# Kernel tuning notes

Measured on AMD Instinct MI355X. Metric: run time of the kernel, lower is better.

The kernel has to match this reference:

```python
import jax, jax.numpy as jnp
import numpy as np

N_NODES = 50000
N_EDGES = 800000
D = 128
BN_EPS = 1e-5

def setup_inputs() -> dict:
    key = jax.random.key(0)
    k1, k2, k3, k4, k5 = jax.random.split(key, 5)
    features = jax.random.normal(k1, (N_NODES, D), dtype=jnp.float32)
    W = jax.random.normal(k2, (D, D), dtype=jnp.float32) * (1.0 / np.sqrt(D))
    b = jax.random.normal(k3, (D,), dtype=jnp.float32) * 0.01
    gamma = jnp.ones((D,), dtype=jnp.float32)
    beta = jnp.zeros((D,), dtype=jnp.float32)
    edge_src = jax.random.randint(k4, (N_EDGES,), 0, N_NODES, dtype=jnp.int32)
    edge_dst = jax.random.randint(k5, (N_EDGES,), 0, N_NODES, dtype=jnp.int32)
    return {"features": features, "W": W, "b": b, "gamma": gamma,
            "beta": beta, "edge_src": edge_src, "edge_dst": edge_dst}

def reference(features, W, b, gamma, beta, edge_src, edge_dst):
    h_in = features
    # in-degrees per node, clamped to >= 1
    degs = jax.ops.segment_sum(jnp.ones_like(edge_dst, dtype=jnp.float32),
                               edge_dst, num_segments=N_NODES)
    norm = jnp.clip(degs, 1.0, None) ** -0.5  # [N]
    norm = norm[:, None]                       # [N, 1]
    # symmetric-norm GCN: scale, copy_src + sum reduce, linear apply, scale
    x = features * norm
    agg = jax.ops.segment_sum(x[edge_src], edge_dst, num_segments=N_NODES)  # [N, D]
    h = agg @ W.T + b
    h = h * norm
    # BatchNorm1d (training-mode math: batch stats over nodes, biased var)
    mean = jnp.mean(h, axis=0)
    var = jnp.mean((h - mean) ** 2, axis=0)
    h = (h - mean) * jax.lax.rsqrt(var + BN_EPS) * gamma + beta
    # ReLU activation, residual; dropout is identity in eval
    h = jax.nn.relu(h)
    h = h_in + h
    return h
```

## Files before the change

### kernel.cpp

```cpp
#include <hip/hip_runtime.h>

#define D 128
#define BN_EPS 1e-5f
#define NPART 8
#define NCHUNK 256
#define CAP 64

typedef __attribute__((ext_vector_type(8))) short short8;
typedef __attribute__((ext_vector_type(4))) float f32x4;

__device__ __forceinline__ unsigned short f2bf(float f) {
    unsigned int x = __float_as_uint(f);
    return (unsigned short)((x + 0x7fffu + ((x >> 16) & 1u)) >> 16);
}

__global__ void k_cast(const float4* __restrict__ inA, ushort4* __restrict__ outA, int n4a,
                       const float4* __restrict__ inB, ushort4* __restrict__ outB, int n4b) {
    int i = blockIdx.x * 256 + threadIdx.x;
    const float4* in; ushort4* out; int k;
    if (i < n4a) { in = inA; out = outA; k = i; }
    else { k = i - n4a; if (k >= n4b) return; in = inB; out = outB; }
    float4 v = in[k];
    ushort4 o;
    o.x = f2bf(v.x); o.y = f2bf(v.y); o.z = f2bf(v.z); o.w = f2bf(v.w);
    out[k] = o;
}

__global__ void p_bucket(const int* __restrict__ src, const int* __restrict__ dst,
                         int* __restrict__ cnt, unsigned short* __restrict__ srcs,
                         int nE, int PS, int CH) {
    int p = blockIdx.x & (NPART - 1);
    int c = blockIdx.x >> 3;
    unsigned lo = (unsigned)(p * PS);
    int e0 = c * CH;
    int e1 = min(e0 + CH, nE);
    for (int e = e0 + threadIdx.x; e < e1; e += 512) {
        int ea = e, eb = e + 256;
        int d0 = dst[ea];
        int d1 = (eb < e1) ? dst[eb] : 0;
        bool a0 = (unsigned)d0 - lo < (unsigned)PS;
        bool a1 = (eb < e1) && ((unsigned)d1 - lo < (unsigned)PS);
        int s0 = a0 ? atomicAdd(&cnt[d0], 1) : CAP;
        int s1 = a1 ? atomicAdd(&cnt[d1], 1) : CAP;
        if (s0 < CAP) srcs[(size_t)d0 * CAP + s0] = (unsigned short)src[ea];
        if (s1 < CAP) srcs[(size_t)d1 * CAP + s1] = (unsigned short)src[eb];
    }
}

template <bool FB>
__global__ __launch_bounds__(256) void k_gather(const int* __restrict__ cnt,
                                                const unsigned short* __restrict__ srcs,
                                                const void* __restrict__ featp,
                                                unsigned int* __restrict__ aggout,
                                                int nN) {
    int node = (blockIdx.x * 256 + threadIdx.x) >> 5;
    if (node >= nN) return;
    int l = threadIdx.x & 31;

    int end = cnt[node];
    if (end > CAP) end = CAP;
    const unsigned short* sl = srcs + (size_t)node * CAP;

    float a0 = 0.0f, a1 = 0.0f, a2 = 0.0f, a3 = 0.0f;
    int i = 0;

    if (FB) {
        const uint2* fb = (const uint2*)featp + l;
        for (; i + 3 < end; i += 4) {
            int s0 = sl[i], s1 = sl[i + 1], s2 = sl[i + 2], s3 = sl[i + 3];
            float n0 = rsqrtf(fmaxf((float)cnt[s0], 1.0f));
            float n1 = rsqrtf(fmaxf((float)cnt[s1], 1.0f));
            float n2 = rsqrtf(fmaxf((float)cnt[s2], 1.0f));
            float n3 = rsqrtf(fmaxf((float)cnt[s3], 1.0f));
            uint2 u0 = fb[(size_t)s0 * 32], u1 = fb[(size_t)s1 * 32];
            uint2 u2 = fb[(size_t)s2 * 32], u3 = fb[(size_t)s3 * 32];
            a0 += __uint_as_float(u0.x << 16) * n0 + __uint_as_float(u1.x << 16) * n1
                + __uint_as_float(u2.x << 16) * n2 + __uint_as_float(u3.x << 16) * n3;
            a1 += __uint_as_float(u0.x & 0xffff0000u) * n0 + __uint_as_float(u1.x & 0xffff0000u) * n1
                + __uint_as_float(u2.x & 0xffff0000u) * n2 + __uint_as_float(u3.x & 0xffff0000u) * n3;
            a2 += __uint_as_float(u0.y << 16) * n0 + __uint_as_float(u1.y << 16) * n1
                + __uint_as_float(u2.y << 16) * n2 + __uint_as_float(u3.y << 16) * n3;
            a3 += __uint_as_float(u0.y & 0xffff0000u) * n0 + __uint_as_float(u1.y & 0xffff0000u) * n1
                + __uint_as_float(u2.y & 0xffff0000u) * n2 + __uint_as_float(u3.y & 0xffff0000u) * n3;
        }
        for (; i < end; ++i) {
            int s = sl[i];
            float n = rsqrtf(fmaxf((float)cnt[s], 1.0f));
            uint2 u = fb[(size_t)s * 32];
            a0 += __uint_as_float(u.x << 16) * n;
            a1 += __uint_as_float(u.x & 0xffff0000u) * n;
            a2 += __uint_as_float(u.y << 16) * n;
            a3 += __uint_as_float(u.y & 0xffff0000u) * n;
        }
    } else {
        const float4* fb = (const float4*)featp + l;
        for (; i + 3 < end; i += 4) {
            int s0 = sl[i], s1 = sl[i + 1], s2 = sl[i + 2], s3 = sl[i + 3];
            float n0 = rsqrtf(fmaxf((float)cnt[s0], 1.0f));
            float n1 = rsqrtf(fmaxf((float)cnt[s1], 1.0f));
            float n2 = rsqrtf(fmaxf((float)cnt[s2], 1.0f));
            float n3 = rsqrtf(fmaxf((float)cnt[s3], 1.0f));
            float4 f0 = fb[(size_t)s0 * 32], f1 = fb[(size_t)s1 * 32];
            float4 f2 = fb[(size_t)s2 * 32], f3 = fb[(size_t)s3 * 32];
            a0 += f0.x * n0 + f1.x * n1 + f2.x * n2 + f3.x * n3;
            a1 += f0.y * n0 + f1.y * n1 + f2.y * n2 + f3.y * n3;
            a2 += f0.z * n0 + f1.z * n1 + f2.z * n2 + f3.z * n3;
            a3 += f0.w * n0 + f1.w * n1 + f2.w * n2 + f3.w * n3;
        }
        for (; i < end; ++i) {
            int s = sl[i];
            float n = rsqrtf(fmaxf((float)cnt[s], 1.0f));
            float4 f = fb[(size_t)s * 32];
            a0 += f.x * n; a1 += f.y * n; a2 += f.z * n; a3 += f.w * n;
        }
    }
    uint2 packed;
    packed.x = (unsigned int)f2bf(a0) | ((unsigned int)f2bf(a1) << 16);
    packed.y = (unsigned int)f2bf(a2) | ((unsigned int)f2bf(a3) << 16);
    ((uint2*)aggout)[(size_t)node * 64 + 32 + l] = packed;
}

__global__ __launch_bounds__(256) void k_gemm(
        const unsigned short* __restrict__ Adata,
        const unsigned short* __restrict__ Wbf,
        const float* __restrict__ b,
        const int* __restrict__ cnt,
        float* __restrict__ h,
        float* __restrict__ colsum, float* __restrict__ colsq,
        int nN) {
    const int tid = threadIdx.x;
    const int lane = tid & 63;
    const int wv = tid >> 6;
    const int wcol0 = wv * 32;
    const int l15 = lane & 15;
    const int lq = lane >> 4;
    const int row0 = blockIdx.x * 64;

    short8 bfrag[2][4];
    #pragma unroll
    for (int ct = 0; ct < 2; ++ct) {
        int n = wcol0 + ct * 16 + l15;
        #pragma unroll
        for (int kc = 0; kc < 4; ++kc)
            bfrag[ct][kc] = *(const short8*)(Wbf + n * 128 + kc * 32 + lq * 8);
    }
    const float bc0 = b[wcol0 + l15], bc1 = b[wcol0 + 16 + l15];

    short8 afrag[4][4];
    #pragma unroll
    for (int rt = 0; rt < 4; ++rt) {
        int arow = row0 + rt * 16 + l15;
        int arc = arow < nN ? arow : (nN - 1);
        #pragma unroll
        for (int kc = 0; kc < 4; ++kc)
            afrag[rt][kc] = *(const short8*)(Adata + (size_t)arc * 256 + 128 + kc * 32 + lq * 8);
    }
    __syncthreads();

    float s1[2] = {0.0f, 0.0f}, s2[2] = {0.0f, 0.0f};

    #pragma unroll
    for (int rt = 0; rt < 4; ++rt) {
        int r0 = row0 + rt * 16;
        f32x4 acc0 = {0.0f, 0.0f, 0.0f, 0.0f};
        f32x4 acc1 = {0.0f, 0.0f, 0.0f, 0.0f};
        #pragma unroll
        for (int kc = 0; kc < 4; ++kc) {
            acc0 = __builtin_amdgcn_mfma_f32_16x16x32_bf16(afrag[rt][kc], bfrag[0][kc], acc0, 0, 0, 0);
            acc1 = __builtin_amdgcn_mfma_f32_16x16x32_bf16(afrag[rt][kc], bfrag[1][kc], acc1, 0, 0, 0);
        }

        #pragma unroll
        for (int reg = 0; reg < 4; ++reg) {
            int row = r0 + lq * 4 + reg;
            if (row < nN) {
                float nm = rsqrtf(fmaxf((float)cnt[row], 1.0f));
                float v0 = (acc0[reg] + bc0) * nm;
                float v1 = (acc1[reg] + bc1) * nm;
                h[(size_t)row * 128 + wcol0 + l15] = v0;
                h[(size_t)row * 128 + wcol0 + 16 + l15] = v1;
                s1[0] += v0; s2[0] += v0 * v0;
                s1[1] += v1; s2[1] += v1 * v1;
            }
        }
    }

    #pragma unroll
    for (int ct = 0; ct < 2; ++ct) {
        s1[ct] += __shfl_xor(s1[ct], 16, 64);
        s1[ct] += __shfl_xor(s1[ct], 32, 64);
        s2[ct] += __shfl_xor(s2[ct], 16, 64);
        s2[ct] += __shfl_xor(s2[ct], 32, 64);
    }
    if (lane < 16) {
        atomicAdd(&colsum[wcol0 + lane], s1[0]);
        atomicAdd(&colsq [wcol0 + lane], s2[0]);
        atomicAdd(&colsum[wcol0 + 16 + lane], s1[1]);
        atomicAdd(&colsq [wcol0 + 16 + lane], s2[1]);
    }
}

__global__ __launch_bounds__(256) void k_bn_out(const float* __restrict__ colsum,
                                                const float* __restrict__ colsq,
                                                const float* __restrict__ gamma,
                                                const float* __restrict__ beta,
                                                float* __restrict__ h,
                                                const float* __restrict__ feat,
                                                float inv_n, int total4) {
    __shared__ float sc[128], sh[128];
    int tid = threadIdx.x;
    if (tid < 128) {
        float mean = colsum[tid] * inv_n;
        float var = colsq[tid] * inv_n - mean * mean;
        float s = gamma[tid] * rsqrtf(var + BN_EPS);
        sc[tid] = s;
        sh[tid] = beta[tid] - mean * s;
    }
    __syncthreads();
    int t = blockIdx.x * 256 + tid;
    if (t >= total4) return;
    int base = t * 4;
    int j = base & 127;
    float4 hv = *(const float4*)(h + base);
    float4 fv = *(const float4*)(feat + base);
    float4 o;
    o.x = fv.x + fmaxf(hv.x * sc[j + 0] + sh[j + 0], 0.0f);
    o.y = fv.y + fmaxf(hv.y * sc[j + 1] + sh[j + 1], 0.0f);
    o.z = fv.z + fmaxf(hv.z * sc[j + 2] + sh[j + 2], 0.0f);
    o.w = fv.w + fmaxf(hv.w * sc[j + 3] + sh[j + 3], 0.0f);
    *(float4*)(h + base) = o;
}

extern "C" void kernel_launch(void* const* d_in, const int* in_sizes, int n_in,
                              void* d_out, int out_size, void* d_ws, size_t ws_size,
                              hipStream_t stream) {
    const float* feat  = (const float*)d_in[0];
    const float* W     = (const float*)d_in[1];
    const float* b     = (const float*)d_in[2];
    const float* gamma = (const float*)d_in[3];
    const float* beta  = (const float*)d_in[4];
    const int* esrc = (const int*)d_in[5];
    const int* edst = (const int*)d_in[6];

    const int nN = in_sizes[0] / D;
    const int nE = in_sizes[5];
    const int PS = (nN + NPART - 1) / NPART;
    const int CH = (nE + NCHUNK - 1) / NCHUNK;

    float* h = (float*)d_out;

    unsigned short* Wbf    = (unsigned short*)d_ws;
    unsigned short* srcs   = Wbf + 128 * 128;
    int*            cnt    = (int*)(srcs + (size_t)nN * CAP);
    float*          colsum = (float*)(cnt + nN);
    float*          colsq  = colsum + 128;
    unsigned short* featbf = (unsigned short*)(colsq + 128);

    size_t need_full = (size_t)((char*)(featbf + (size_t)nN * D) - (char*)d_ws);
    bool useFB = ws_size >= need_full;

    hipMemsetAsync(cnt, 0, ((size_t)nN + 256) * sizeof(int), stream);

    int n4a = 128 * 128 / 4;
    int n4b = useFB ? nN * D / 4 : 0;
    k_cast<<<(n4a + n4b + 255) / 256, 256, 0, stream>>>(
        (const float4*)W, (ushort4*)Wbf, n4a,
        (const float4*)feat, (ushort4*)featbf, n4b);

    p_bucket<<<NPART * NCHUNK, 256, 0, stream>>>(esrc, edst, cnt, srcs, nE, PS, CH);

    int gblocks = (nN * 32 + 255) / 256;
    if (useFB)
        k_gather<true><<<gblocks, 256, 0, stream>>>(cnt, srcs, featbf, (unsigned int*)d_out, nN);
    else
        k_gather<false><<<gblocks, 256, 0, stream>>>(cnt, srcs, feat, (unsigned int*)d_out, nN);

    k_gemm<<<(nN + 63) / 64, 256, 0, stream>>>((const unsigned short*)d_out, Wbf, b, cnt,
                                               h, colsum, colsq, nN);

    int total4 = nN * D / 4;
    k_bn_out<<<(total4 + 255) / 256, 256, 0, stream>>>(colsum, colsq, gamma, beta,
                                                       h, feat, 1.0f / (float)nN, total4);
}
```

Measured before the change: 211.9 us.

## Fuse GEMM with BatchNorm via cooperative grid sync; merge cast and bucket kernels

Adds a cooperative kernel that computes the GEMM, keeps the normalized h tile in registers, and accumulates column stats with atomics. After a grid-wide sync it applies BatchNorm, ReLU and the residual directly. This avoids writing h to memory and reading it back in a separate pass. The cast and edge-bucketing kernels are merged into one launch, and bucketing is unrolled to four edges per thread. The grid barrier needs all blocks resident at once, and the old two-kernel path is kept as a fallback if that can't be met.

```diff
diff --git a/kernel.cpp b/kernel.cpp
--- a/kernel.cpp
+++ b/kernel.cpp
@@ -1,10 +1,14 @@
 #include <hip/hip_runtime.h>
+#include <hip/hip_cooperative_groups.h>
+
+namespace cg = cooperative_groups;
 
 #define D 128
 #define BN_EPS 1e-5f
 #define NPART 8
 #define NCHUNK 256
 #define CAP 64
+#define NUM_CU 256
 
 typedef __attribute__((ext_vector_type(8))) short short8;
 typedef __attribute__((ext_vector_type(4))) float f32x4;
@@ -14,36 +18,47 @@
     return (unsigned short)((x + 0x7fffu + ((x >> 16) & 1u)) >> 16);
 }
 
-__global__ void k_cast(const float4* __restrict__ inA, ushort4* __restrict__ outA, int n4a,
-                       const float4* __restrict__ inB, ushort4* __restrict__ outB, int n4b) {
-    int i = blockIdx.x * 256 + threadIdx.x;
-    const float4* in; ushort4* out; int k;
-    if (i < n4a) { in = inA; out = outA; k = i; }
-    else { k = i - n4a; if (k >= n4b) return; in = inB; out = outB; }
-    float4 v = in[k];
-    ushort4 o;
-    o.x = f2bf(v.x); o.y = f2bf(v.y); o.z = f2bf(v.z); o.w = f2bf(v.w);
-    out[k] = o;
-}
-
-__global__ void p_bucket(const int* __restrict__ src, const int* __restrict__ dst,
-                         int* __restrict__ cnt, unsigned short* __restrict__ srcs,
-                         int nE, int PS, int CH) {
-    int p = blockIdx.x & (NPART - 1);
-    int c = blockIdx.x >> 3;
-    unsigned lo = (unsigned)(p * PS);
-    int e0 = c * CH;
-    int e1 = min(e0 + CH, nE);
-    for (int e = e0 + threadIdx.x; e < e1; e += 512) {
-        int ea = e, eb = e + 256;
-        int d0 = dst[ea];
-        int d1 = (eb < e1) ? dst[eb] : 0;
-        bool a0 = (unsigned)d0 - lo < (unsigned)PS;
-        bool a1 = (eb < e1) && ((unsigned)d1 - lo < (unsigned)PS);
-        int s0 = a0 ? atomicAdd(&cnt[d0], 1) : CAP;
-        int s1 = a1 ? atomicAdd(&cnt[d1], 1) : CAP;
-        if (s0 < CAP) srcs[(size_t)d0 * CAP + s0] = (unsigned short)src[ea];
-        if (s1 < CAP) srcs[(size_t)d1 * CAP + s1] = (unsigned short)src[eb];
+__global__ __launch_bounds__(256) void k_prep(
+        const int* __restrict__ src, const int* __restrict__ dst,
+        int* __restrict__ cnt, unsigned short* __restrict__ srcs,
+        int nE, int PS, int CH,
+        const float4* __restrict__ inA, ushort4* __restrict__ outA, int n4a,
+        const float4* __restrict__ inB, ushort4* __restrict__ outB, int n4b) {
+    int bid = blockIdx.x;
+    if (bid < NPART * NCHUNK) {
+        int p = bid & (NPART - 1);
+        int c = bid >> 3;
+        unsigned lo = (unsigned)(p * PS);
+        int e0 = c * CH;
+        int e1 = min(e0 + CH, nE);
+        for (int e = e0 + (int)threadIdx.x; e < e1; e += 1024) {
+            int ea = e, eb = e + 256, ec = e + 512, ed = e + 768;
+            int d0 = dst[ea];
+            int d1 = (eb < e1) ? dst[eb] : 0;
+            int d2 = (ec < e1) ? dst[ec] : 0;
+            int d3 = (ed < e1) ? dst[ed] : 0;
+            bool a0 = (unsigned)d0 - lo < (unsigned)PS;
+            bool a1 = (eb < e1) && ((unsigned)d1 - lo < (unsigned)PS);
+            bool a2 = (ec < e1) && ((unsigned)d2 - lo < (unsigned)PS);
+            bool a3 = (ed < e1) && ((unsigned)d3 - lo < (unsigned)PS);
+            int s0 = a0 ? atomicAdd(&cnt[d0], 1) : CAP;
+            int s1 = a1 ? atomicAdd(&cnt[d1], 1) : CAP;
+            int s2 = a2 ? atomicAdd(&cnt[d2], 1) : CAP;
+            int s3 = a3 ? atomicAdd(&cnt[d3], 1) : CAP;
+            if (s0 < CAP) srcs[(size_t)d0 * CAP + s0] = (unsigned short)src[ea];
+            if (s1 < CAP) srcs[(size_t)d1 * CAP + s1] = (unsigned short)src[eb];
+            if (s2 < CAP) srcs[(size_t)d2 * CAP + s2] = (unsigned short)src[ec];
+            if (s3 < CAP) srcs[(size_t)d3 * CAP + s3] = (unsigned short)src[ed];
+        }
+    } else {
+        int i = (bid - NPART * NCHUNK) * 256 + threadIdx.x;
+        const float4* in; ushort4* out; int k;
+        if (i < n4a) { in = inA; out = outA; k = i; }
+        else { k = i - n4a; if (k >= n4b) return; in = inB; out = outB; }
+        float4 v = in[k];
+        ushort4 o;
+        o.x = f2bf(v.x); o.y = f2bf(v.y); o.z = f2bf(v.z); o.w = f2bf(v.w);
+        out[k] = o;
     }
 }
 
@@ -120,6 +135,110 @@
     ((uint2*)aggout)[(size_t)node * 64 + 32 + l] = packed;
 }
 
+__global__ __launch_bounds__(256, 4) void k_gemm_bn(
+        const unsigned short* __restrict__ Adata,
+        const unsigned short* __restrict__ Wbf,
+        const float* __restrict__ bvec,
+        const int* __restrict__ cnt,
+        float* __restrict__ colsum, float* __restrict__ colsq,
+        const float* __restrict__ gamma, const float* __restrict__ beta,
+        const float* __restrict__ feat,
+        float* __restrict__ out,
+        int nN, float inv_n) {
+    const int tid = threadIdx.x;
+    const int lane = tid & 63;
+    const int wv = tid >> 6;
+    const int wcol0 = wv * 32;
+    const int l15 = lane & 15;
+    const int lq = lane >> 4;
+    const int row0 = blockIdx.x * 64;
+
+    short8 bfrag[2][4];
+    #pragma unroll
+    for (int ct = 0; ct < 2; ++ct) {
+        int n = wcol0 + ct * 16 + l15;
+        #pragma unroll
+        for (int kc = 0; kc < 4; ++kc)
+            bfrag[ct][kc] = *(const short8*)(Wbf + n * 128 + kc * 32 + lq * 8);
+    }
+    const float bc0 = bvec[wcol0 + l15], bc1 = bvec[wcol0 + 16 + l15];
+
+    float hv0[4][4], hv1[4][4];
+    float s1[2] = {0.0f, 0.0f}, s2[2] = {0.0f, 0.0f};
+
+    #pragma unroll
+    for (int rt = 0; rt < 4; ++rt) {
+        int arow = row0 + rt * 16 + l15;
+        int arc = arow < nN ? arow : (nN - 1);
+        short8 af[4];
+        #pragma unroll
+        for (int kc = 0; kc < 4; ++kc)
+            af[kc] = *(const short8*)(Adata + (size_t)arc * 256 + 128 + kc * 32 + lq * 8);
+
+        f32x4 acc0 = {0.0f, 0.0f, 0.0f, 0.0f};
+        f32x4 acc1 = {0.0f, 0.0f, 0.0f, 0.0f};
+        #pragma unroll
+        for (int kc = 0; kc < 4; ++kc) {
+            acc0 = __builtin_amdgcn_mfma_f32_16x16x32_bf16(af[kc], bfrag[0][kc], acc0, 0, 0, 0);
+            acc1 = __builtin_amdgcn_mfma_f32_16x16x32_bf16(af[kc], bfrag[1][kc], acc1, 0, 0, 0);
+        }
+
+        #pragma unroll
+        for (int reg = 0; reg < 4; ++reg) {
+            int row = row0 + rt * 16 + lq * 4 + reg;
+            float nm = 0.0f;
+            if (row < nN) nm = rsqrtf(fmaxf((float)cnt[row], 1.0f));
+            float v0 = (acc0[reg] + bc0) * nm;
+            float v1 = (acc1[reg] + bc1) * nm;
+            hv0[rt][reg] = v0;
+            hv1[rt][reg] = v1;
+            if (row < nN) {
+                s1[0] += v0; s2[0] += v0 * v0;
+                s1[1] += v1; s2[1] += v1 * v1;
+            }
+        }
+    }
+
+    #pragma unroll
+    for (int ct = 0; ct < 2; ++ct) {
+        s1[ct] += __shfl_xor(s1[ct], 16, 64);
+        s1[ct] += __shfl_xor(s1[ct], 32, 64);
+        s2[ct] += __shfl_xor(s2[ct], 16, 64);
+        s2[ct] += __shfl_xor(s2[ct], 32, 64);
+    }
+    if (lane < 16) {
+        atomicAdd(&colsum[wcol0 + lane], s1[0]);
+        atomicAdd(&colsq [wcol0 + lane], s2[0]);
+        atomicAdd(&colsum[wcol0 + 16 + lane], s1[1]);
+        atomicAdd(&colsq [wcol0 + 16 + lane], s2[1]);
+    }
+
+    cg::this_grid().sync();
+
+    const int c0 = wcol0 + l15, c1 = wcol0 + 16 + l15;
+    float m0 = colsum[c0] * inv_n, m1 = colsum[c1] * inv_n;
+    float va0 = colsq[c0] * inv_n - m0 * m0;
+    float va1 = colsq[c1] * inv_n - m1 * m1;
+    float sc0 = gamma[c0] * rsqrtf(va0 + BN_EPS);
+    float sc1 = gamma[c1] * rsqrtf(va1 + BN_EPS);
+    float sh0 = beta[c0] - m0 * sc0;
+    float sh1 = beta[c1] - m1 * sc1;
+
+    #pragma unroll
+    for (int rt = 0; rt < 4; ++rt) {
+        #pragma unroll
+        for (int reg = 0; reg < 4; ++reg) {
+            int row = row0 + rt * 16 + lq * 4 + reg;
+            if (row < nN) {
+                size_t o0 = (size_t)row * 128 + c0;
+                size_t o1 = (size_t)row * 128 + c1;
+                out[o0] = feat[o0] + fmaxf(hv0[rt][reg] * sc0 + sh0, 0.0f);
+                out[o1] = feat[o1] + fmaxf(hv1[rt][reg] * sc1 + sh1, 0.0f);
+            }
+        }
+    }
+}
+
 __global__ __launch_bounds__(256) void k_gemm(
         const unsigned short* __restrict__ Adata,
         const unsigned short* __restrict__ Wbf,
@@ -169,7 +288,6 @@
             acc0 = __builtin_amdgcn_mfma_f32_16x16x32_bf16(afrag[rt][kc], bfrag[0][kc], acc0, 0, 0, 0);
             acc1 = __builtin_amdgcn_mfma_f32_16x16x32_bf16(afrag[rt][kc], bfrag[1][kc], acc1, 0, 0, 0);
         }
-
         #pragma unroll
         for (int reg = 0; reg < 4; ++reg) {
             int row = r0 + lq * 4 + reg;
@@ -263,11 +381,11 @@
 
     int n4a = 128 * 128 / 4;
     int n4b = useFB ? nN * D / 4 : 0;
-    k_cast<<<(n4a + n4b + 255) / 256, 256, 0, stream>>>(
+    int castBlocks = (n4a + n4b + 255) / 256;
+    k_prep<<<NPART * NCHUNK + castBlocks, 256, 0, stream>>>(
+        esrc, edst, cnt, srcs, nE, PS, CH,
         (const float4*)W, (ushort4*)Wbf, n4a,
         (const float4*)feat, (ushort4*)featbf, n4b);
-
-    p_bucket<<<NPART * NCHUNK, 256, 0, stream>>>(esrc, edst, cnt, srcs, nE, PS, CH);
 
     int gblocks = (nN * 32 + 255) / 256;
     if (useFB)
@@ -275,10 +393,35 @@
     else
         k_gather<false><<<gblocks, 256, 0, stream>>>(cnt, srcs, feat, (unsigned int*)d_out, nN);
 
-    k_gemm<<<(nN + 63) / 64, 256, 0, stream>>>((const unsigned short*)d_out, Wbf, b, cnt,
-                                               h, colsum, colsq, nN);
-
-    int total4 = nN * D / 4;
-    k_bn_out<<<(total4 + 255) / 256, 256, 0, stream>>>(colsum, colsq, gamma, beta,
-                                                       h, feat, 1.0f / (float)nN, total4);
-}
+    int gb = (nN + 63) / 64;
+    float inv_n = 1.0f / (float)nN;
+
+    static int coop = -1;
+    if (coop < 0) {
+        int nb = 0;
+        if (hipOccupancyMaxActiveBlocksPerMultiprocessor(&nb, (const void*)k_gemm_bn, 256, 0)
+                != hipSuccess) nb = 0;
+        coop = (nb * NUM_CU >= gb) ? 1 : 0;
+        (void)hipGetLastError();
+    }
+
+    bool done = false;
+    if (coop) {
+        const unsigned short* Adata = (const unsigned short*)d_out;
+        int nN_ = nN;
+        void* cargs[] = {(void*)&Adata, (void*)&Wbf, (void*)&b, (void*)&cnt,
+                         (void*)&colsum, (void*)&colsq, (void*)&gamma, (void*)&beta,
+                         (void*)&feat, (void*)&h, (void*)&nN_, (void*)&inv_n};
+        hipError_t err = hipLaunchCooperativeKernel((const void*)k_gemm_bn,
+                                                    dim3(gb), dim3(256), cargs, 0, stream);
+        if (err == hipSuccess) done = true;
+        else (void)hipGetLastError();
+    }
+    if (!done) {
+        k_gemm<<<gb, 256, 0, stream>>>((const unsigned short*)d_out, Wbf, b, cnt,
+                                       h, colsum, colsq, nN);
+        int total4 = nN * D / 4;
+        k_bn_out<<<(total4 + 255) / 256, 256, 0, stream>>>(colsum, colsq, gamma, beta,
+                                                           h, feat, inv_n, total4);
+    }
+}
```

Result: no change. 208.2 us, median of 2 (-1.8%).
